# Performance work log

Hardware: AMD Instinct MI355X
Metric: run time of the kernel (lower is better)

## Reference

```python
import jax, jax.numpy as jnp
import numpy as np

ALPHA = 1.5   # entmax alpha (module init arg)
N_ITER = 50   # bisection iterations (EntmaxBisect default in this repo)


def _entmax_bisect(X):
    """alpha-entmax over last dim via bisection; faithful to EntmaxBisectFunction.forward."""
    a = ALPHA
    Xs = X * (a - 1.0)
    d = Xs.shape[-1]
    max_val = jnp.max(Xs, axis=-1, keepdims=True)
    tau_lo = max_val - 1.0                      # _gp(1, alpha) == 1
    tau_hi = max_val - (1.0 / d) ** (a - 1.0)   # _gp(1/d, alpha)

    def p(tau):  # _p: clamp then ** (1/(alpha-1))
        return jnp.clip(Xs - tau, 0.0) ** (1.0 / (a - 1.0))

    f_lo = jnp.sum(p(tau_lo), axis=-1, keepdims=True) - 1.0
    dm0 = tau_hi - tau_lo

    def body(i, carry):
        tau_lo, dm, _ = carry
        dm = dm * 0.5
        tau_m = tau_lo + dm
        f_m = jnp.sum(p(tau_m), axis=-1, keepdims=True) - 1.0
        mask = (f_m * f_lo) >= 0.0
        tau_lo = jnp.where(mask, tau_m, tau_lo)
        return (tau_lo, dm, tau_m)

    _, _, tau_m = jax.lax.fori_loop(0, N_ITER, body, (tau_lo, dm0, tau_lo))
    P = p(tau_m)
    return P / jnp.sum(P, axis=-1, keepdims=True)  # ensure_sum_one


def setup_inputs() -> dict:
    key = jax.random.key(0)
    k0, k1, k2, k3 = jax.random.split(key, 4)
    B, R = 1, 4096
    NFIELD, NEMB, H = 65, 256, 8
    HD, DK = NEMB // H, NEMB
    x = jax.random.normal(k0, (B, R, NFIELD * NEMB), dtype=jnp.float32)
    # xavier-ish scales for the learned params
    bilinear_w = jax.random.normal(k1, (H, HD, DK), dtype=jnp.float32) * 0.15
    query = jax.random.normal(k2, (H, DK), dtype=jnp.float32) * 0.15
    values = jax.random.normal(k3, (H, NFIELD - 1), dtype=jnp.float32) * 0.3
    return {"x": x, "bilinear_w": bilinear_w, "query": query, "values": values}


def reference(x, bilinear_w, query, values):
    # x: [1, R, nfield*nemb]  (leading dim must be 1; torch.squeeze in source assumes it)
    B, R, D = x.shape
    h, dk = query.shape
    nemb = dk               # d_k == nemb in ExponentialNeuron
    nfield = D // nemb
    hd = nemb // h
    scale = nemb ** -0.5

    xr = x.reshape(R, nfield, nemb)                       # squeeze b=1: [R, f, e]
    # rearrange 'b r c (h hd) -> h r c hd' (b squeezed)
    keys = xr[:, 1:, :].reshape(R, nfield - 1, h, hd).transpose(2, 0, 1, 3)
    # att_gates: einsum('h r c d, h d k, h k -> h r c') * scale
    att = jnp.einsum('hrcd,hdk,hk->hrc', keys, bilinear_w, query) * scale
    gates = _entmax_bisect(att)                           # [h, R, c]
    cross_weight = gates * values[:, None, :]             # einsum('hbf,hf->hbf')
    # x_cross = exp(einsum('bfe,hbf->bhe'))
    x_cross = jnp.exp(jnp.einsum('rfe,hrf->rhe', xr[:, 1:, :], cross_weight))
    x_cross = x_cross.reshape(B, R, h * nemb)
    return jnp.concatenate([x, x_cross], axis=-1)         # [1, R, (nfield+h)*nemb]
```

## Files before the change

### kernel.cpp

```cpp
#include <hip/hip_runtime.h>
#include <math.h>

namespace {

constexpr int kRows = 4096;
constexpr int kNF   = 65;
constexpr int kNE   = 256;
constexpr int kNH   = 8;
constexpr int kNC   = 64;
constexpr int kXRow = kNF * kNE;
constexpr int kORow = (kNF + kNH) * kNE;

typedef float vf4 __attribute__((ext_vector_type(4)));

__device__ __forceinline__ void nt_store4(const float4& v, float4* dst) {
  vf4 t = {v.x, v.y, v.z, v.w};
  __builtin_nontemporal_store(t, reinterpret_cast<vf4*>(dst));
}

__global__ __launch_bounds__(256) void w2_precompute(
    const float* __restrict__ bw, const float* __restrict__ query,
    float* __restrict__ w2) {
  const int o = threadIdx.x >> 5;
  const int l = threadIdx.x & 31;
  const int t = blockIdx.x * 8 + o;
  const int h = t >> 5;
  const float4* __restrict__ bp =
      reinterpret_cast<const float4*>(bw + (size_t)t * 256 + l * 8);
  const float4* __restrict__ qp =
      reinterpret_cast<const float4*>(query + (size_t)h * 256 + l * 8);
  const float4 b0 = bp[0], b1 = bp[1];
  const float4 q0 = qp[0], q1 = qp[1];
  float acc = b0.x * q0.x + b0.y * q0.y + b0.z * q0.z + b0.w * q0.w
            + b1.x * q1.x + b1.y * q1.y + b1.z * q1.z + b1.w * q1.w;
  acc += __shfl_xor(acc, 1);
  acc += __shfl_xor(acc, 2);
  acc += __shfl_xor(acc, 4);
  acc += __shfl_xor(acc, 8);
  acc += __shfl_xor(acc, 16);
  if (l == 0) w2[t] = acc;
}

__global__ __launch_bounds__(512) void fused_row(
    const float* __restrict__ x, const float* __restrict__ w2g,
    const float* __restrict__ vals, float* __restrict__ out) {
  __shared__ float att_t[kNC * 9];
  __shared__ float cw[kNC * kNH];
  __shared__ float4 part[8 * 4 * 64];

  const int tid  = threadIdx.x;
  const int wv   = tid >> 6;
  const int lane = tid & 63;
  const int r    = blockIdx.x;

  const float* __restrict__ xrow = x + (size_t)r * kXRow;
  float* __restrict__ orow       = out + (size_t)r * kORow;
  const float4* __restrict__ x4  = reinterpret_cast<const float4*>(xrow);
  float4* __restrict__ o4        = reinterpret_cast<float4*>(orow);

  float4 kreg[8];
  const float4 wq = reinterpret_cast<const float4*>(w2g)[lane];
  float4 v0;
  if (wv == 0) v0 = x4[lane];
#pragma unroll
  for (int j = 0; j < 8; ++j) {
    kreg[j] = x4[(wv * 8 + j + 1) * 64 + lane];
  }
  if (wv == 0) nt_store4(v0, &o4[lane]);
#pragma unroll
  for (int j = 0; j < 8; ++j) {
    const int c = wv * 8 + j;
    const float4 v = kreg[j];
    nt_store4(v, &o4[(c + 1) * 64 + lane]);
    float p = v.x * wq.x + v.y * wq.y + v.z * wq.z + v.w * wq.w;
    p += __shfl_xor(p, 1);
    p += __shfl_xor(p, 2);
    p += __shfl_xor(p, 4);
    if ((lane & 7) == 0) att_t[c * 9 + (lane >> 3)] = p * 0.03125f;
  }
  __syncthreads();

  {
    const int h  = lane >> 3;
    const int kk = lane & 7;
    float X[8];
#pragma unroll
    for (int j = 0; j < 8; ++j) X[j] = att_t[(kk * 8 + j) * 9 + h];

    float mx = X[0];
#pragma unroll
    for (int j = 1; j < 8; ++j) mx = fmaxf(mx, X[j]);
    mx = fmaxf(mx, __shfl_xor(mx, 1));
    mx = fmaxf(mx, __shfl_xor(mx, 2));
    mx = fmaxf(mx, __shfl_xor(mx, 4));

    float tau = mx - 1.0f;
    for (int it = 0; it < 16; ++it) {
      float s2 = 0.f, s1 = 0.f;
#pragma unroll
      for (int j = 0; j < 8; ++j) {
        const float t = fmaxf(X[j] - tau, 0.f);
        s2 += t * t;
        s1 += t;
      }
      s2 += __shfl_xor(s2, 1); s1 += __shfl_xor(s1, 1);
      s2 += __shfl_xor(s2, 2); s1 += __shfl_xor(s1, 2);
      s2 += __shfl_xor(s2, 4); s1 += __shfl_xor(s1, 4);
      const float delta = (s2 - 1.0f) / (2.0f * fmaxf(s1, 1e-30f));
      const float ntau = tau + delta;
      if (__all(ntau == tau)) break;
      tau = ntau;
    }

    float s = 0.f;
    float p[8];
#pragma unroll
    for (int j = 0; j < 8; ++j) {
      const float t = fmaxf(X[j] - tau, 0.f);
      p[j] = t * t;
      s += p[j];
    }
    s += __shfl_xor(s, 1);
    s += __shfl_xor(s, 2);
    s += __shfl_xor(s, 4);
    const float inv = 1.0f / s;
    const float* __restrict__ vrow = vals + h * kNC + kk * 8;
#pragma unroll
    for (int j = 0; j < 8; ++j) {
      cw[(kk * 8 + j) * kNH + h] = p[j] * inv * vrow[j];
    }
  }

  const float4* __restrict__ cw4 = reinterpret_cast<const float4*>(cw);
  const float* partf             = reinterpret_cast<const float*>(part);
#pragma unroll
  for (int hh = 0; hh < 2; ++hh) {
    float4 a0 = make_float4(0.f, 0.f, 0.f, 0.f);
    float4 a1 = make_float4(0.f, 0.f, 0.f, 0.f);
    float4 a2 = make_float4(0.f, 0.f, 0.f, 0.f);
    float4 a3 = make_float4(0.f, 0.f, 0.f, 0.f);
#pragma unroll
    for (int j = 0; j < 8; ++j) {
      const float4 kv = kreg[j];
      const float4 ca = cw4[(wv * 8 + j) * 2 + hh];
      a0.x += ca.x * kv.x; a0.y += ca.x * kv.y; a0.z += ca.x * kv.z; a0.w += ca.x * kv.w;
      a1.x += ca.y * kv.x; a1.y += ca.y * kv.y; a1.z += ca.y * kv.z; a1.w += ca.y * kv.w;
      a2.x += ca.z * kv.x; a2.y += ca.z * kv.y; a2.z += ca.z * kv.z; a2.w += ca.z * kv.w;
      a3.x += ca.w * kv.x; a3.y += ca.w * kv.y; a3.z += ca.w * kv.z; a3.w += ca.w * kv.w;
    }
    part[wv * 256 + 0 * 64 + lane] = a0;
    part[wv * 256 + 1 * 64 + lane] = a1;
    part[wv * 256 + 2 * 64 + lane] = a2;
    part[wv * 256 + 3 * 64 + lane] = a3;
    __syncthreads();
#pragma unroll
    for (int oo = 0; oo < 2; ++oo) {
      const int o = oo * 512 + tid;
      float s = partf[o];
#pragma unroll
      for (int sl = 1; sl < 8; ++sl) s += partf[sl * 1024 + o];
      __builtin_nontemporal_store(__expf(s), &orow[kXRow + hh * 1024 + o]);
    }
    if (hh == 0) __syncthreads();
  }
}

}

extern "C" void kernel_launch(void* const* d_in, const int* in_sizes, int n_in,
                              void* d_out, int out_size, void* d_ws, size_t ws_size,
                              hipStream_t stream) {
  const float* x     = reinterpret_cast<const float*>(d_in[0]);
  const float* bw    = reinterpret_cast<const float*>(d_in[1]);
  const float* query = reinterpret_cast<const float*>(d_in[2]);
  const float* vals  = reinterpret_cast<const float*>(d_in[3]);
  float* out = reinterpret_cast<float*>(d_out);
  float* w2  = reinterpret_cast<float*>(d_ws);

  hipLaunchKernelGGL(w2_precompute, dim3(32), dim3(256), 0, stream, bw, query, w2);
  hipLaunchKernelGGL(fused_row, dim3(kRows), dim3(512), 0, stream, x, w2, vals, out);
}
```

Measured before the change: 107.6 us.

## Halve block size to 256 threads and re-load key rows instead of holding them

The fused row kernel now runs with 4 waves per row instead of 8. Each wave handles 16 fields, loaded in two batches of 8, instead of keeping 8 float4 rows live in registers. In the gating phase the key data is re-read from global memory (likely hitting cache) rather than kept in registers. The att_t scratch is aliased onto the part buffer, with an extra barrier, to cut LDS use. The final reduction now uses float4 loads and stores. The aim is higher occupancy and lower register and LDS pressure, at the cost of reloading x and doing more serial work per thread.

```diff
diff --git a/kernel.cpp b/kernel.cpp
--- a/kernel.cpp
+++ b/kernel.cpp
@@ -41,12 +41,12 @@
   if (l == 0) w2[t] = acc;
 }
 
-__global__ __launch_bounds__(512) void fused_row(
+__global__ __launch_bounds__(256) void fused_row(
     const float* __restrict__ x, const float* __restrict__ w2g,
     const float* __restrict__ vals, float* __restrict__ out) {
-  __shared__ float att_t[kNC * 9];
   __shared__ float cw[kNC * kNH];
-  __shared__ float4 part[8 * 4 * 64];
+  __shared__ float4 part[4 * 4 * 64];
+  float* att_t = reinterpret_cast<float*>(part);
 
   const int tid  = threadIdx.x;
   const int wv   = tid >> 6;
@@ -58,25 +58,28 @@
   const float4* __restrict__ x4  = reinterpret_cast<const float4*>(xrow);
   float4* __restrict__ o4        = reinterpret_cast<float4*>(orow);
 
-  float4 kreg[8];
   const float4 wq = reinterpret_cast<const float4*>(w2g)[lane];
   float4 v0;
   if (wv == 0) v0 = x4[lane];
 #pragma unroll
-  for (int j = 0; j < 8; ++j) {
-    kreg[j] = x4[(wv * 8 + j + 1) * 64 + lane];
-  }
-  if (wv == 0) nt_store4(v0, &o4[lane]);
+  for (int b = 0; b < 2; ++b) {
+    float4 buf[8];
 #pragma unroll
-  for (int j = 0; j < 8; ++j) {
-    const int c = wv * 8 + j;
-    const float4 v = kreg[j];
-    nt_store4(v, &o4[(c + 1) * 64 + lane]);
-    float p = v.x * wq.x + v.y * wq.y + v.z * wq.z + v.w * wq.w;
-    p += __shfl_xor(p, 1);
-    p += __shfl_xor(p, 2);
-    p += __shfl_xor(p, 4);
-    if ((lane & 7) == 0) att_t[c * 9 + (lane >> 3)] = p * 0.03125f;
+    for (int j = 0; j < 8; ++j) {
+      buf[j] = x4[(wv * 16 + b * 8 + j + 1) * 64 + lane];
+    }
+    if (b == 0 && wv == 0) nt_store4(v0, &o4[lane]);
+#pragma unroll
+    for (int j = 0; j < 8; ++j) {
+      const int c = wv * 16 + b * 8 + j;
+      const float4 v = buf[j];
+      nt_store4(v, &o4[(c + 1) * 64 + lane]);
+      float p = v.x * wq.x + v.y * wq.y + v.z * wq.z + v.w * wq.w;
+      p += __shfl_xor(p, 1);
+      p += __shfl_xor(p, 2);
+      p += __shfl_xor(p, 4);
+      if ((lane & 7) == 0) att_t[c * 9 + (lane >> 3)] = p * 0.03125f;
+    }
   }
   __syncthreads();
 
@@ -86,6 +89,7 @@
     float X[8];
 #pragma unroll
     for (int j = 0; j < 8; ++j) X[j] = att_t[(kk * 8 + j) * 9 + h];
+    __syncthreads();
 
     float mx = X[0];
 #pragma unroll
@@ -132,7 +136,6 @@
   }
 
   const float4* __restrict__ cw4 = reinterpret_cast<const float4*>(cw);
-  const float* partf             = reinterpret_cast<const float*>(part);
 #pragma unroll
   for (int hh = 0; hh < 2; ++hh) {
     float4 a0 = make_float4(0.f, 0.f, 0.f, 0.f);
@@ -140,26 +143,37 @@
     float4 a2 = make_float4(0.f, 0.f, 0.f, 0.f);
     float4 a3 = make_float4(0.f, 0.f, 0.f, 0.f);
 #pragma unroll
-    for (int j = 0; j < 8; ++j) {
-      const float4 kv = kreg[j];
-      const float4 ca = cw4[(wv * 8 + j) * 2 + hh];
-      a0.x += ca.x * kv.x; a0.y += ca.x * kv.y; a0.z += ca.x * kv.z; a0.w += ca.x * kv.w;
-      a1.x += ca.y * kv.x; a1.y += ca.y * kv.y; a1.z += ca.y * kv.z; a1.w += ca.y * kv.w;
-      a2.x += ca.z * kv.x; a2.y += ca.z * kv.y; a2.z += ca.z * kv.z; a2.w += ca.z * kv.w;
-      a3.x += ca.w * kv.x; a3.y += ca.w * kv.y; a3.z += ca.w * kv.z; a3.w += ca.w * kv.w;
+    for (int b = 0; b < 2; ++b) {
+      float4 kb[8];
+#pragma unroll
+      for (int j = 0; j < 8; ++j) {
+        kb[j] = x4[(wv * 16 + b * 8 + j + 1) * 64 + lane];
+      }
+#pragma unroll
+      for (int j = 0; j < 8; ++j) {
+        const float4 kv = kb[j];
+        const float4 ca = cw4[(wv * 16 + b * 8 + j) * 2 + hh];
+        a0.x += ca.x * kv.x; a0.y += ca.x * kv.y; a0.z += ca.x * kv.z; a0.w += ca.x * kv.w;
+        a1.x += ca.y * kv.x; a1.y += ca.y * kv.y; a1.z += ca.y * kv.z; a1.w += ca.y * kv.w;
+        a2.x += ca.z * kv.x; a2.y += ca.z * kv.y; a2.z += ca.z * kv.z; a2.w += ca.z * kv.w;
+        a3.x += ca.w * kv.x; a3.y += ca.w * kv.y; a3.z += ca.w * kv.z; a3.w += ca.w * kv.w;
+      }
     }
     part[wv * 256 + 0 * 64 + lane] = a0;
     part[wv * 256 + 1 * 64 + lane] = a1;
     part[wv * 256 + 2 * 64 + lane] = a2;
     part[wv * 256 + 3 * 64 + lane] = a3;
     __syncthreads();
+    {
+      float4 s = part[tid];
 #pragma unroll
-    for (int oo = 0; oo < 2; ++oo) {
-      const int o = oo * 512 + tid;
-      float s = partf[o];
-#pragma unroll
-      for (int sl = 1; sl < 8; ++sl) s += partf[sl * 1024 + o];
-      __builtin_nontemporal_store(__expf(s), &orow[kXRow + hh * 1024 + o]);
+      for (int sl = 1; sl < 4; ++sl) {
+        const float4 t = part[sl * 256 + tid];
+        s.x += t.x; s.y += t.y; s.z += t.z; s.w += t.w;
+      }
+      float4 e;
+      e.x = __expf(s.x); e.y = __expf(s.y); e.z = __expf(s.z); e.w = __expf(s.w);
+      nt_store4(e, &reinterpret_cast<float4*>(orow + kXRow + hh * 1024)[tid]);
     }
     if (hh == 0) __syncthreads();
   }
@@ -178,5 +192,5 @@
   float* w2  = reinterpret_cast<float*>(d_ws);
 
   hipLaunchKernelGGL(w2_precompute, dim3(32), dim3(256), 0, stream, bw, query, w2);
-  hipLaunchKernelGGL(fused_row, dim3(kRows), dim3(512), 0, stream, x, w2, vals, out);
+  hipLaunchKernelGGL(fused_row, dim3(kRows), dim3(256), 0, stream, x, w2, vals, out);
 }
```

Result: slower. 135.4 us (+25.8%).
